# Kernel tuning notes

Hardware: AMD Instinct MI355X
Metric: run time of the kernel (lower is better)

## Reference

```python
import jax, jax.numpy as jnp
import numpy as np

NEG = -1e9  # effective -inf in log space (finite to keep grads NaN-free)


def _forward_lattice(theta, A):
    """alpha[b,i,j,s]: log-prob of all alignments reaching cell (i,j) in state s.
    States: 0=match (diag move), 1=insert-x (down move), 2=insert-y (right move).
    alpha[i,j,s] = theta[i,j,s] + LSE_k(alpha[i-ds,j-dj,k] + A[k,s]).
    Start: only the match contribution at (0,0) gets log-prob 0."""
    B, N, M, S = theta.shape
    j_is0 = (jnp.arange(M) == 0)  # [M]

    def row_step(prev_row, xs):
        theta_row, i = xs  # theta_row: [B, M, S]
        # diag predecessor alpha[i-1, j-1, :]
        diag = jnp.concatenate(
            [jnp.full((B, 1, S), NEG, theta_row.dtype), prev_row[:, :-1]], axis=1)
        lse_m = jax.nn.logsumexp(diag + A[:, None, :, 0], axis=-1)      # [B, M]
        lse_m = jnp.where((i == 0) & j_is0[None, :], 0.0, lse_m)        # start at (0,0)
        lse_x = jax.nn.logsumexp(prev_row + A[:, None, :, 1], axis=-1)  # [B, M]
        m_vals = theta_row[:, :, 0] + lse_m
        x_vals = theta_row[:, :, 1] + lse_x
        th_y = theta_row[:, :, 2]

        def col_step(left, cxs):
            # left: alpha[i, j-1, :] -> [B, S]
            m_j, x_j, ty_j = cxs  # each [B]
            y_j = ty_j + jax.nn.logsumexp(left + A[:, :, 2], axis=-1)
            cell = jnp.stack([m_j, x_j, y_j], axis=-1)  # [B, S]
            return cell, cell

        left0 = jnp.full((B, S), NEG, theta_row.dtype)
        _, row = jax.lax.scan(col_step, left0, (m_vals.T, x_vals.T, th_y.T))
        row = jnp.transpose(row, (1, 0, 2))  # [B, M, S]
        return row, row

    prev0 = jnp.full((B, M, S), NEG, theta.dtype)
    _, alpha = jax.lax.scan(row_step, prev0, (jnp.swapaxes(theta, 0, 1), jnp.arange(N)))
    return jnp.swapaxes(alpha, 0, 1)  # [B, N, M, S]


def _backward_lattice(theta, A):
    """beta[b,i,j,s]: log-prob of all alignment suffixes from (i,j) in state s.
    beta[i,j,s] = LSE( A[s,0]+theta[i+1,j+1,0]+beta[i+1,j+1,0],
                       A[s,1]+theta[i+1,j,1]  +beta[i+1,j,1],
                       A[s,2]+theta[i,j+1,2]  +beta[i,j+1,2] ),  beta[N-1,M-1,:] = 0.
    Computed as a forward scan on the flipped grid with u = beta + theta."""
    B, N, M, S = theta.shape
    theta_f = theta[:, ::-1, ::-1]
    j_is0 = (jnp.arange(M) == 0)

    def row_step(u_prev, xs):
        th_row, p = xs  # th_row: [B, M, S] (flipped coords)
        t_m = jnp.concatenate(
            [jnp.full((B, 1), NEG, th_row.dtype), u_prev[:, :-1, 0]], axis=1)  # [B, M]
        t_x = u_prev[:, :, 1]  # [B, M]

        def col_step(left_u2, cxs):
            tm_j, tx_j, th_j, j0 = cxs  # [B], [B], [B,S], scalar bool
            v = jnp.stack([tm_j, tx_j, left_u2], axis=-1)     # [B, S] over successor k
            g = jax.nn.logsumexp(A + v[:, None, :], axis=-1)  # [B, S]
            g = jnp.where((p == 0) & j0, 0.0, g)              # terminal cell
            u = g + th_j
            return u[:, 2], (g, u)

        left0 = jnp.full((B,), NEG, th_row.dtype)
        _, (g_row, u_row) = jax.lax.scan(
            col_step, left0, (t_m.T, t_x.T, jnp.swapaxes(th_row, 0, 1), j_is0))
        return jnp.transpose(u_row, (1, 0, 2)), jnp.transpose(g_row, (1, 0, 2))

    u0 = jnp.full((B, M, S), NEG, theta.dtype)
    _, g = jax.lax.scan(row_step, u0, (jnp.swapaxes(theta_f, 0, 1), jnp.arange(N)))
    g = jnp.swapaxes(g, 0, 1)  # [B, N, M, S] flipped coords
    return g[:, ::-1, ::-1]


def setup_inputs() -> dict:
    key = jax.random.key(0)
    k1, k2 = jax.random.split(key)
    B, N, M, S = 256, 128, 128, 3
    theta = jax.random.normal(k1, (B, N, M, S), dtype=jnp.float32)
    A = jax.random.normal(k2, (B, S, S), dtype=jnp.float32)
    return {"theta": theta, "A": A}


def reference(theta, A):
    # Baum-Welch: posterior log-marginals gamma = alpha + beta - logZ
    alpha = _forward_lattice(theta, A)
    beta = _backward_lattice(theta, A)
    logZ = jax.nn.logsumexp(alpha[:, -1, -1, :], axis=-1)  # [B]
    return alpha + beta - logZ[:, None, None, None]
```

## Files before the change

kernel.cpp:

```cpp
#include <hip/hip_runtime.h>

#define HNEG (-1000000000.0f)

constexpr int Nc = 128;
constexpr int Mc = 128;
constexpr int CELLS = Nc * Mc * 3;

__device__ __host__ constexpr int dpoff(int d) {
  return d <= 128 ? (d * (d + 1)) / 2 + ((d + 1) >> 1)
                  : 16448 - ((255 - d) * (256 - d)) / 2 + ((d - 127) >> 1);
}
__device__ __forceinline__ int dlod(int d) { return d > 127 ? d - 127 : 0; }
__device__ __forceinline__ int sidx(int d, int j) {
  const int lo = dlod(d);
  return dpoff(d) + j - lo + (lo & 1);
}
constexpr int PCELLS = 16512;
constexpr int PFLOATS = PCELLS * 3;
constexpr int AWSTRIDE = CELLS + 16;

__device__ __forceinline__ float lse3(float a, float b, float c) {
  float mx = fmaxf(fmaxf(a, b), c);
  return mx + __logf(__expf(a - mx) + __expf(b - mx) + __expf(c - mx));
}

__device__ __forceinline__ float shr1f(float src, float fill) {
  return __int_as_float(__builtin_amdgcn_update_dpp(
      __float_as_int(fill), __float_as_int(src), 0x138, 0xF, 0xF, false));
}

__device__ __forceinline__ void st3_even(float* o, float a, float b, float c) {
  *(float2*)o = make_float2(a, b);
  o[2] = c;
}
__device__ __forceinline__ void st3_odd(float* o, float a, float b, float c) {
  o[0] = a;
  *(float2*)(o + 1) = make_float2(b, c);
}

__global__ __launch_bounds__(256) void transpose_kernel(
    const float* __restrict__ theta, float* __restrict__ thd) {
  const int b = blockIdx.x;
  const int tile = blockIdx.y;
  const int i0 = (tile >> 1) * 64, j0 = (tile & 1) * 64;
  const int t = threadIdx.x;
  __shared__ float lds[64 * 192];
  float4* lds4 = (float4*)lds;
  const float4* src4 = (const float4*)(theta + (size_t)b * CELLS);
  float* dst = thd + (size_t)b * PFLOATS;
  const int cbase = (j0 >> 6) * 48;
  for (int f = t; f < 64 * 48; f += 256) {
    const int r = f / 48, c4 = f - r * 48;
    lds4[f] = src4[(size_t)(i0 + r) * 96 + cbase + c4];
  }
  __syncthreads();
  const int g = t >> 6, w = t & 63;
  for (int ld = g; ld < 127; ld += 4) {
    const int d = i0 + j0 + ld;
    const int ljlo = ld > 63 ? ld - 63 : 0;
    const int ljhi = ld < 63 ? ld : 63;
    const int L = (ljhi - ljlo + 1) * 3;
    const int base = sidx(d, j0 + ljlo) * 3;
    for (int e = w; e < L; e += 64) {
      const int lj = ljlo + e / 3, s = e - (e / 3) * 3;
      dst[base + e] = lds[(ld - lj) * 192 + lj * 3 + s];
    }
  }
}

#define DECL6(p) float p##0, p##1, p##2, p##3, p##4, p##5


#define F2LOAD(P, dd) do {                                                     \
    const int dc_ = (dd) > 254 ? 254 : (dd);                                   \
    const float2* p2_ = (const float2*)(thd + (size_t)sidx(dc_, jA) * 3);      \
    const float2 la_ = p2_[0], lb_ = p2_[1], lc_ = p2_[2];                     \
    P##0 = la_.x; P##1 = la_.y; P##2 = lb_.x;                                  \
    P##3 = lb_.y; P##4 = lc_.x; P##5 = lc_.y;                                  \
  } while (0)

#define F2STEP(P, dd) do {                                                     \
    const int iA_ = (dd) - jA, iB_ = (dd) - jB;                                \
    const bool okA_ = (unsigned)iA_ < (unsigned)Nc;                            \
    const bool okB_ = (unsigned)iB_ < (unsigned)Nc;                            \
    const float g0 = mS2 + __logf(wS20 * E00 + wS21 * E10 + wS22 * E20);       \
    const float g1 = mPA + __logf(wPA0 * E01 + wPA1 * E11 + wPA2 * E21);       \
    const float g2 = mS1 + __logf(wS10 * E02 + wS11 * E12 + wS12 * E22);       \
    const float cA0 = okA_ ? P##0 + g0 : HNEG;                                 \
    const float cA1 = okA_ ? P##1 + g1 : HNEG;                                 \
    const float cA2 = okA_ ? P##2 + g2 : HNEG;                                 \
    st3_even(okA_ ? aw + (iA_ * Mc + jA) * 3 : dmpE, cA0, cA1, cA2);           \
    const float h0 = mPP + __logf(wPP0 * E00 + wPP1 * E10 + wPP2 * E20);       \
    const float h1 = mPB + __logf(wPB0 * E01 + wPB1 * E11 + wPB2 * E21);       \
    const float h2 = mPA + __logf(wPA0 * E02 + wPA1 * E12 + wPA2 * E22);       \
    const float cB0 = okB_ ? P##3 + h0 : HNEG;                                 \
    const float cB1 = okB_ ? P##4 + h1 : HNEG;                                 \
    const float cB2 = okB_ ? P##5 + h2 : HNEG;                                 \
    st3_odd(okB_ ? aw + (iB_ * Mc + jB) * 3 : dmpO, cB0, cB1, cB2);            \
    const float mA_ = fmaxf(fmaxf(cA0, cA1), cA2);                             \
    const float a0_ = __expf(cA0 - mA_), a1_ = __expf(cA1 - mA_),              \
                a2_ = __expf(cA2 - mA_);                                       \
    const float mB_ = fmaxf(fmaxf(cB0, cB1), cB2);                             \
    const float b0_ = __expf(cB0 - mB_), b1_ = __expf(cB1 - mB_),              \
                b2_ = __expf(cB2 - mB_);                                       \
    mPP = mPA; wPP0 = wPA0; wPP1 = wPA1; wPP2 = wPA2;                          \
    mPA = mA_; wPA0 = a0_; wPA1 = a1_; wPA2 = a2_;                             \
    mPB = mB_; wPB0 = b0_; wPB1 = b1_; wPB2 = b2_;                             \
    mS2 = mS1; wS20 = wS10; wS21 = wS11; wS22 = wS12;                          \
    mS1 = shr1f(mB_, HNEG);                                                    \
    wS10 = shr1f(b0_, 1.f); wS11 = shr1f(b1_, 1.f); wS12 = shr1f(b2_, 1.f);    \
  } while (0)

#define B2LOADL(Pt, dd) do {                                                   \
    int dor_ = 254 - (dd); if (dor_ < 0) dor_ = 0;                             \
    const float2* p2_ = (const float2*)(thd + (size_t)sidx(dor_, jjB) * 3);    \
    const float2 la_ = p2_[0], lb_ = p2_[1], lc_ = p2_[2];                     \
    Pt##3 = la_.x; Pt##4 = la_.y; Pt##5 = lb_.x;                               \
    Pt##0 = lb_.y; Pt##1 = lc_.x; Pt##2 = lc_.y;                               \
  } while (0)

#define B2STEPL(Pt, dd) do {                                                   \
    const int iA_ = Nc - 1 - (dd) + jA;                                        \
    const int iB_ = Nc - 1 - (dd) + jB;                                        \
    const bool okA_ = (unsigned)iA_ < (unsigned)Nc;                            \
    const bool okB_ = (unsigned)iB_ < (unsigned)Nc;                            \
    float uA0, uA1, uA2, uB0, uB1, uB2;                                        \
    {                                                                          \
      const float v0 = S2u0, v1 = pAu1, v2 = S1u2;                             \
      const float mv = fmaxf(fmaxf(v0, v1), v2);                               \
      const float w0 = __expf(v0 - mv), w1 = __expf(v1 - mv),                  \
                  w2 = __expf(v2 - mv);                                        \
      float g0 = mv + __logf(w0 * E00 + w1 * E01 + w2 * E02);                  \
      float g1 = mv + __logf(w0 * E10 + w1 * E11 + w2 * E12);                  \
      float g2 = mv + __logf(w0 * E20 + w1 * E21 + w2 * E22);                  \
      if ((dd) == 0 && l == 0) { g0 = 0.f; g1 = 0.f; g2 = 0.f; }               \
      uA0 = okA_ ? g0 + Pt##0 : HNEG;                                          \
      uA1 = okA_ ? g1 + Pt##1 : HNEG;                                          \
      uA2 = okA_ ? g2 + Pt##2 : HNEG;                                          \
      st3_odd(okA_ ? ob + (iA_ * Mc + jjA) * 3 : dmpO, g0, g1, g2);            \
    }                                                                          \
    {                                                                          \
      const float v0 = ppAu0, v1 = pBu1, v2 = pAu2;                            \
      const float mv = fmaxf(fmaxf(v0, v1), v2);                               \
      const float w0 = __expf(v0 - mv), w1 = __expf(v1 - mv),                  \
                  w2 = __expf(v2 - mv);                                        \
      const float g0 = mv + __logf(w0 * E00 + w1 * E01 + w2 * E02);            \
      const float g1 = mv + __logf(w0 * E10 + w1 * E11 + w2 * E12);            \
      const float g2 = mv + __logf(w0 * E20 + w1 * E21 + w2 * E22);            \
      uB0 = okB_ ? g0 + Pt##3 : HNEG;                                          \
      uB1 = okB_ ? g1 + Pt##4 : HNEG;                                          \
      uB2 = okB_ ? g2 + Pt##5 : HNEG;                                          \
      st3_even(okB_ ? ob + (iB_ * Mc + jjB) * 3 : dmpE, g0, g1, g2);           \
    }                                                                          \
    ppAu0 = pAu0; pAu0 = uA0; pAu1 = uA1; pAu2 = uA2; pBu1 = uB1;              \
    S2u0 = S1u0;                                                               \
    S1u0 = shr1f(uB0, HNEG);                                                   \
    S1u2 = shr1f(uB2, HNEG);                                                   \
  } while (0)

__global__ __launch_bounds__(128, 1) void fb2_kernel(
    const float* __restrict__ thd_, const float* __restrict__ A,
    float* __restrict__ aw_, float* __restrict__ logZ_ws,
    float* __restrict__ ob_) {
  const int b = blockIdx.x;
  const int wave = threadIdx.x >> 6;
  const int l = threadIdx.x & 63;
  const float* thd = thd_ + (size_t)b * PFLOATS;
  const float* Ab = A + b * 9;
  const float E00 = __expf(Ab[0]), E01 = __expf(Ab[1]), E02 = __expf(Ab[2]);
  const float E10 = __expf(Ab[3]), E11 = __expf(Ab[4]), E12 = __expf(Ab[5]);
  const float E20 = __expf(Ab[6]), E21 = __expf(Ab[7]), E22 = __expf(Ab[8]);

  const int jA = 2 * l, jB = 2 * l + 1;
  float* dpad = aw_ + (size_t)b * AWSTRIDE + CELLS;

  if (wave == 0) {
    float* aw = aw_ + (size_t)b * AWSTRIDE;
    float* dmpE = dpad;
    float* dmpO = dpad + 3;

    float mPA = HNEG, wPA0 = 1.f, wPA1 = 1.f, wPA2 = 1.f;
    float mPB = HNEG, wPB0 = 1.f, wPB1 = 1.f, wPB2 = 1.f;
    float mPP = HNEG, wPP0 = 1.f, wPP1 = 1.f, wPP2 = 1.f;
    float mS1 = HNEG, wS10 = 1.f, wS11 = 1.f, wS12 = 1.f;
    float mS2 = HNEG, wS20 = 1.f, wS21 = 1.f, wS22 = 1.f;
    if (l == 0) { mS2 = 0.f; wS20 = 1.0f / E00; wS21 = 0.f; wS22 = 0.f; }

    DECL6(xt0); DECL6(xt1); DECL6(xt2); DECL6(xt3);
    DECL6(yt0); DECL6(yt1); DECL6(yt2); DECL6(yt3);

    F2LOAD(xt0, 0); F2LOAD(xt1, 1); F2LOAD(xt2, 2); F2LOAD(xt3, 3);
    F2LOAD(yt0, 4); F2LOAD(yt1, 5); F2LOAD(yt2, 6); F2LOAD(yt3, 7);

    for (int t = 0; t < 31; ++t) {
      const int d0 = 8 * t;
      F2STEP(xt0, d0 + 0); F2STEP(xt1, d0 + 1); F2STEP(xt2, d0 + 2); F2STEP(xt3, d0 + 3);
      F2LOAD(xt0, d0 + 8); F2LOAD(xt1, d0 + 9); F2LOAD(xt2, d0 + 10); F2LOAD(xt3, d0 + 11);
      F2STEP(yt0, d0 + 4); F2STEP(yt1, d0 + 5); F2STEP(yt2, d0 + 6); F2STEP(yt3, d0 + 7);
      F2LOAD(yt0, d0 + 12); F2LOAD(yt1, d0 + 13); F2LOAD(yt2, d0 + 14); F2LOAD(yt3, d0 + 15);
    }
    F2STEP(xt0, 248); F2STEP(xt1, 249); F2STEP(xt2, 250); F2STEP(xt3, 251);
    F2STEP(yt0, 252); F2STEP(yt1, 253); F2STEP(yt2, 254);
    if (l == 63) logZ_ws[b] = mPB + __logf(wPB0 + wPB1 + wPB2);
  } else {
    float* ob = ob_ + (size_t)b * CELLS;
    const int jjA = Mc - 1 - jA, jjB = Mc - 1 - jB;
    float* dmpE = dpad + 8;
    float* dmpO = dpad + 11;

    float pAu0 = HNEG, pAu1 = HNEG, pAu2 = HNEG;
    float ppAu0 = HNEG, pBu1 = HNEG;
    float S1u0 = HNEG, S1u2 = HNEG, S2u0 = HNEG;

    DECL6(xt0); DECL6(xt1); DECL6(xt2); DECL6(xt3);
    DECL6(yt0); DECL6(yt1); DECL6(yt2); DECL6(yt3);

    B2LOADL(xt0, 0); B2LOADL(xt1, 1); B2LOADL(xt2, 2); B2LOADL(xt3, 3);
    B2LOADL(yt0, 4); B2LOADL(yt1, 5); B2LOADL(yt2, 6); B2LOADL(yt3, 7);

    for (int t = 0; t < 31; ++t) {
      const int d0 = 8 * t;
      B2STEPL(xt0, d0 + 0); B2STEPL(xt1, d0 + 1);
      B2STEPL(xt2, d0 + 2); B2STEPL(xt3, d0 + 3);
      B2LOADL(xt0, d0 + 8); B2LOADL(xt1, d0 + 9);
      B2LOADL(xt2, d0 + 10); B2LOADL(xt3, d0 + 11);
      B2STEPL(yt0, d0 + 4); B2STEPL(yt1, d0 + 5);
      B2STEPL(yt2, d0 + 6); B2STEPL(yt3, d0 + 7);
      B2LOADL(yt0, d0 + 12); B2LOADL(yt1, d0 + 13);
      B2LOADL(yt2, d0 + 14); B2LOADL(yt3, d0 + 15);
    }
    B2STEPL(xt0, 248); B2STEPL(xt1, 249); B2STEPL(xt2, 250); B2STEPL(xt3, 251);
    B2STEPL(yt0, 252); B2STEPL(yt1, 253); B2STEPL(yt2, 254);
  }
}

__global__ __launch_bounds__(256) void combine_kernel(
    const float4* __restrict__ aw4, const float* __restrict__ logZ_ws,
    float4* __restrict__ out4) {
  const int b = blockIdx.x;
  const float lz = logZ_ws[b];
  const int off = blockIdx.y * 1024 + threadIdx.x;
  const size_t ab = (size_t)b * (AWSTRIDE / 4);
  const size_t obx = (size_t)b * 12288;
#pragma unroll
  for (int k = 0; k < 4; ++k) {
    const size_t i = off + (size_t)k * 256;
    const float4 a = aw4[ab + i];
    const float4 g = out4[obx + i];
    out4[obx + i] = make_float4(a.x + g.x - lz, a.y + g.y - lz,
                                a.z + g.z - lz, a.w + g.w - lz);
  }
}

__global__ __launch_bounds__(128) void fwd_fb(const float* __restrict__ theta,
                                              const float* __restrict__ A,
                                              float* __restrict__ out) {
  const int b = blockIdx.x;
  const int j = threadIdx.x;
  const float* th = theta + (size_t)b * CELLS;
  float* ob = out + (size_t)b * CELLS;

  __shared__ float sA[9];
  __shared__ float ring[3][Mc + 1][3];
  if (j < 9) sA[j] = A[b * 9 + j];
  {
    float* rf = &ring[0][0][0];
    for (int t = j; t < 3 * (Mc + 1) * 3; t += Mc) rf[t] = HNEG;
  }
  __syncthreads();
  const float A00 = sA[0], A01 = sA[1], A02 = sA[2];
  const float A10 = sA[3], A11 = sA[4], A12 = sA[5];
  const float A20 = sA[6], A21 = sA[7], A22 = sA[8];

  float p0 = HNEG, p1 = HNEG, p2 = HNEG;
  float tc0 = 0.f, tc1 = 0.f, tc2 = 0.f, tn0 = 0.f, tn1 = 0.f, tn2 = 0.f;
  if (j == 0) { tc0 = th[0]; tc1 = th[1]; tc2 = th[2]; }
  if (j <= 1) {
    const int i1 = 1 - j;
    const float* p = th + (i1 * Mc + j) * 3;
    tn0 = p[0]; tn1 = p[1]; tn2 = p[2];
  }
  int s0 = 0, s1 = 2, s2 = 1;
  for (int d = 0; d < Nc + Mc - 1; ++d) {
    const int i = d - j;
    float tf0 = 0.f, tf1 = 0.f, tf2 = 0.f;
    const int ip = i + 2;
    if (ip >= 0 && ip < Nc) {
      const float* p = th + (ip * Mc + j) * 3;
      tf0 = p[0]; tf1 = p[1]; tf2 = p[2];
    }
    float c0 = HNEG, c1 = HNEG, c2 = HNEG;
    if (i >= 0 && i < Nc) {
      const float* nd1 = ring[s1][j];
      const float* nd2 = ring[s2][j];
      float lm = lse3(nd2[0] + A00, nd2[1] + A10, nd2[2] + A20);
      if (i == 0 && j == 0) lm = 0.0f;
      float lx = lse3(p0 + A01, p1 + A11, p2 + A21);
      float ly = lse3(nd1[0] + A02, nd1[1] + A12, nd1[2] + A22);
      c0 = tc0 + lm; c1 = tc1 + lx; c2 = tc2 + ly;
      float* o = ob + (i * Mc + j) * 3;
      o[0] = c0; o[1] = c1; o[2] = c2;
    }
    float* w = ring[s0][j + 1];
    w[0] = c0; w[1] = c1; w[2] = c2;
    __syncthreads();
    p0 = c0; p1 = c1; p2 = c2;
    tc0 = tn0; tc1 = tn1; tc2 = tn2;
    tn0 = tf0; tn1 = tf1; tn2 = tf2;
    const int t = s2; s2 = s1; s1 = s0; s0 = t;
  }
}

__global__ __launch_bounds__(128) void bwd_fb(const float* __restrict__ theta,
                                              const float* __restrict__ A,
                                              float* __restrict__ ob_) {
  const int b = blockIdx.x;
  const int q = threadIdx.x;
  const float* th = theta + (size_t)b * CELLS;
  float* ob = ob_ + (size_t)b * CELLS;

  __shared__ float sA[9];
  __shared__ float ring[3][Mc + 1][3];
  __shared__ float sZ;
  if (q < 9) sA[q] = A[b * 9 + q];
  {
    float* rf = &ring[0][0][0];
    for (int t = q; t < 3 * (Mc + 1) * 3; t += Mc) rf[t] = HNEG;
  }
  if (q == 0) {
    sZ = lse3(ob[(Nc * Mc - 1) * 3 + 0], ob[(Nc * Mc - 1) * 3 + 1],
              ob[(Nc * Mc - 1) * 3 + 2]);
  }
  __syncthreads();
  const float A00 = sA[0], A01 = sA[1], A02 = sA[2];
  const float A10 = sA[3], A11 = sA[4], A12 = sA[5];
  const float A20 = sA[6], A21 = sA[7], A22 = sA[8];
  const float logZ = sZ;

  const int jj = Mc - 1 - q;
  float pu1 = HNEG;
  float tc0 = 0.f, tc1 = 0.f, tc2 = 0.f, tn0 = 0.f, tn1 = 0.f, tn2 = 0.f;
  float ac0 = 0.f, ac1 = 0.f, ac2 = 0.f, an0 = 0.f, an1 = 0.f, an2 = 0.f;
  if (q == 0) {
    const float* p = th + ((Nc - 1) * Mc + jj) * 3;
    tc0 = p[0]; tc1 = p[1]; tc2 = p[2];
    const float* a = ob + ((Nc - 1) * Mc + jj) * 3;
    ac0 = a[0]; ac1 = a[1]; ac2 = a[2];
  }
  if (q <= 1) {
    const int i1 = Nc - 2 + q;
    const float* p = th + (i1 * Mc + jj) * 3;
    tn0 = p[0]; tn1 = p[1]; tn2 = p[2];
    const float* a = ob + (i1 * Mc + jj) * 3;
    an0 = a[0]; an1 = a[1]; an2 = a[2];
  }
  int s0 = 0, s1 = 2, s2 = 1;
  for (int d = 0; d < Nc + Mc - 1; ++d) {
    const int p = d - q;
    const int i = Nc - 1 - p;
    float tf0 = 0.f, tf1 = 0.f, tf2 = 0.f, af0 = 0.f, af1 = 0.f, af2 = 0.f;
    const int ipf = i - 2;
    if (ipf >= 0 && ipf < Nc) {
      const float* pp = th + (ipf * Mc + jj) * 3;
      tf0 = pp[0]; tf1 = pp[1]; tf2 = pp[2];
      const float* aa = ob + (ipf * Mc + jj) * 3;
      af0 = aa[0]; af1 = aa[1]; af2 = aa[2];
    }
    float u0 = HNEG, u1 = HNEG, u2 = HNEG;
    if (p >= 0 && p < Nc) {
      const float* nd1 = ring[s1][q];
      const float* nd2 = ring[s2][q];
      const float v0 = nd2[0];
      const float v1 = pu1;
      const float v2 = nd1[2];
      float g0 = lse3(A00 + v0, A01 + v1, A02 + v2);
      float g1 = lse3(A10 + v0, A11 + v1, A12 + v2);
      float g2 = lse3(A20 + v0, A21 + v1, A22 + v2);
      if (p == 0 && q == 0) { g0 = 0.0f; g1 = 0.0f; g2 = 0.0f; }
      u0 = g0 + tc0; u1 = g1 + tc1; u2 = g2 + tc2;
      float* o = ob + (i * Mc + jj) * 3;
      o[0] = ac0 + g0 - logZ;
      o[1] = ac1 + g1 - logZ;
      o[2] = ac2 + g2 - logZ;
    }
    float* w = ring[s0][q + 1];
    w[0] = u0; w[1] = u1; w[2] = u2;
    __syncthreads();
    pu1 = u1;
    tc0 = tn0; tc1 = tn1; tc2 = tn2;
    tn0 = tf0; tn1 = tf1; tn2 = tf2;
    ac0 = an0; ac1 = an1; ac2 = an2;
    an0 = af0; an1 = af1; an2 = af2;
    const int t = s2; s2 = s1; s1 = s0; s0 = t;
  }
}

extern "C" void kernel_launch(void* const* d_in, const int* in_sizes, int n_in,
                              void* d_out, int out_size, void* d_ws, size_t ws_size,
                              hipStream_t stream) {
  const float* theta = (const float*)d_in[0];
  const float* A = (const float*)d_in[1];
  float* out = (float*)d_out;
  const int B = in_sizes[1] / 9;

  const size_t need = (size_t)B * (PFLOATS + AWSTRIDE + 1) * 4;
  if (ws_size >= need) {
    float* thd = (float*)d_ws;
    float* aw = thd + (size_t)B * PFLOATS;
    float* logZ_ws = aw + (size_t)B * AWSTRIDE;
    transpose_kernel<<<dim3(B, 4), dim3(256), 0, stream>>>(theta, thd);
    fb2_kernel<<<dim3(B), dim3(128), 0, stream>>>(thd, A, aw, logZ_ws, out);
    combine_kernel<<<dim3(B, 12), dim3(256), 0, stream>>>(
        (const float4*)aw, logZ_ws, (float4*)out);
  } else {
    fwd_fb<<<dim3(B), dim3(128), 0, stream>>>(theta, A, out);
    bwd_fb<<<dim3(B), dim3(128), 0, stream>>>(theta, A, out);
  }
}
```

Measured before the change: 240.3 us.

## Run lattice recurrences in base-2 log space and use uniform theta addressing

The theta repack pre-scales values by 1/ln2, so both forward and backward recurrences can use the native exp2/log2 instructions in place of __expf/__logf, which each carry an extra multiply. The final combine multiplies by ln2 to return to natural log. Theta load addresses are also computed once per wave with readfirstlane plus a per-lane offset, moving index arithmetic to scalar registers. This adds rounding from the scaling and relies on the repack's lane layout matching the per-lane offset.

```diff
diff --git a/kernel.cpp b/kernel.cpp
--- a/kernel.cpp
+++ b/kernel.cpp
@@ -1,10 +1,20 @@
 #include <hip/hip_runtime.h>
 
 #define HNEG (-1000000000.0f)
+#define HNEG2 (-1.44269504e9f)
+#define INVLN2 1.44269504088896341f
+#define LN2F 0.69314718055994531f
 
 constexpr int Nc = 128;
 constexpr int Mc = 128;
 constexpr int CELLS = Nc * Mc * 3;
+
+__device__ __forceinline__ float ex2(float x) {
+  return __builtin_amdgcn_exp2f(x);
+}
+__device__ __forceinline__ float lg2(float x) {
+  return __builtin_amdgcn_logf(x);
+}
 
 __device__ __host__ constexpr int dpoff(int d) {
   return d <= 128 ? (d * (d + 1)) / 2 + ((d + 1) >> 1)
@@ -14,6 +24,10 @@
 __device__ __forceinline__ int sidx(int d, int j) {
   const int lo = dlod(d);
   return dpoff(d) + j - lo + (lo & 1);
+}
+__device__ __forceinline__ int sidx_u(int d) {
+  const int lo = dlod(d);
+  return dpoff(d) - lo + (lo & 1);
 }
 constexpr int PCELLS = 16512;
 constexpr int PFLOATS = PCELLS * 3;
@@ -63,7 +77,7 @@
     const int base = sidx(d, j0 + ljlo) * 3;
     for (int e = w; e < L; e += 64) {
       const int lj = ljlo + e / 3, s = e - (e / 3) * 3;
-      dst[base + e] = lds[(ld - lj) * 192 + lj * 3 + s];
+      dst[base + e] = lds[(ld - lj) * 192 + lj * 3 + s] * INVLN2;
     }
   }
 }
@@ -73,7 +87,8 @@
 
 #define F2LOAD(P, dd) do {                                                     \
     const int dc_ = (dd) > 254 ? 254 : (dd);                                   \
-    const float2* p2_ = (const float2*)(thd + (size_t)sidx(dc_, jA) * 3);      \
+    const int su_ = __builtin_amdgcn_readfirstlane(sidx_u(dc_));               \
+    const float2* p2_ = (const float2*)thd + ((su_ * 3) >> 1) + 3 * l;         \
     const float2 la_ = p2_[0], lb_ = p2_[1], lc_ = p2_[2];                     \
     P##0 = la_.x; P##1 = la_.y; P##2 = lb_.x;                                  \
     P##3 = lb_.y; P##4 = lc_.x; P##5 = lc_.y;                                  \
@@ -83,37 +98,39 @@
     const int iA_ = (dd) - jA, iB_ = (dd) - jB;                                \
     const bool okA_ = (unsigned)iA_ < (unsigned)Nc;                            \
     const bool okB_ = (unsigned)iB_ < (unsigned)Nc;                            \
-    const float g0 = mS2 + __logf(wS20 * E00 + wS21 * E10 + wS22 * E20);       \
-    const float g1 = mPA + __logf(wPA0 * E01 + wPA1 * E11 + wPA2 * E21);       \
-    const float g2 = mS1 + __logf(wS10 * E02 + wS11 * E12 + wS12 * E22);       \
-    const float cA0 = okA_ ? P##0 + g0 : HNEG;                                 \
-    const float cA1 = okA_ ? P##1 + g1 : HNEG;                                 \
-    const float cA2 = okA_ ? P##2 + g2 : HNEG;                                 \
+    const float g0 = mS2 + lg2(wS20 * E00 + wS21 * E10 + wS22 * E20);          \
+    const float g1 = mPA + lg2(wPA0 * E01 + wPA1 * E11 + wPA2 * E21);          \
+    const float g2 = mS1 + lg2(wS10 * E02 + wS11 * E12 + wS12 * E22);          \
+    const float cA0 = okA_ ? P##0 + g0 : HNEG2;                                \
+    const float cA1 = okA_ ? P##1 + g1 : HNEG2;                                \
+    const float cA2 = okA_ ? P##2 + g2 : HNEG2;                                \
     st3_even(okA_ ? aw + (iA_ * Mc + jA) * 3 : dmpE, cA0, cA1, cA2);           \
-    const float h0 = mPP + __logf(wPP0 * E00 + wPP1 * E10 + wPP2 * E20);       \
-    const float h1 = mPB + __logf(wPB0 * E01 + wPB1 * E11 + wPB2 * E21);       \
-    const float h2 = mPA + __logf(wPA0 * E02 + wPA1 * E12 + wPA2 * E22);       \
-    const float cB0 = okB_ ? P##3 + h0 : HNEG;                                 \
-    const float cB1 = okB_ ? P##4 + h1 : HNEG;                                 \
-    const float cB2 = okB_ ? P##5 + h2 : HNEG;                                 \
+    const float h0 = mPP + lg2(wPP0 * E00 + wPP1 * E10 + wPP2 * E20);          \
+    const float h1 = mPB + lg2(wPB0 * E01 + wPB1 * E11 + wPB2 * E21);          \
+    const float h2 = mPA + lg2(wPA0 * E02 + wPA1 * E12 + wPA2 * E22);          \
+    const float cB0 = okB_ ? P##3 + h0 : HNEG2;                                \
+    const float cB1 = okB_ ? P##4 + h1 : HNEG2;                                \
+    const float cB2 = okB_ ? P##5 + h2 : HNEG2;                                \
     st3_odd(okB_ ? aw + (iB_ * Mc + jB) * 3 : dmpO, cB0, cB1, cB2);            \
     const float mA_ = fmaxf(fmaxf(cA0, cA1), cA2);                             \
-    const float a0_ = __expf(cA0 - mA_), a1_ = __expf(cA1 - mA_),              \
-                a2_ = __expf(cA2 - mA_);                                       \
+    const float a0_ = ex2(cA0 - mA_), a1_ = ex2(cA1 - mA_),                    \
+                a2_ = ex2(cA2 - mA_);                                          \
     const float mB_ = fmaxf(fmaxf(cB0, cB1), cB2);                             \
-    const float b0_ = __expf(cB0 - mB_), b1_ = __expf(cB1 - mB_),              \
-                b2_ = __expf(cB2 - mB_);                                       \
+    const float b0_ = ex2(cB0 - mB_), b1_ = ex2(cB1 - mB_),                    \
+                b2_ = ex2(cB2 - mB_);                                          \
     mPP = mPA; wPP0 = wPA0; wPP1 = wPA1; wPP2 = wPA2;                          \
     mPA = mA_; wPA0 = a0_; wPA1 = a1_; wPA2 = a2_;                             \
     mPB = mB_; wPB0 = b0_; wPB1 = b1_; wPB2 = b2_;                             \
     mS2 = mS1; wS20 = wS10; wS21 = wS11; wS22 = wS12;                          \
-    mS1 = shr1f(mB_, HNEG);                                                    \
+    mS1 = shr1f(mB_, HNEG2);                                                   \
     wS10 = shr1f(b0_, 1.f); wS11 = shr1f(b1_, 1.f); wS12 = shr1f(b2_, 1.f);    \
   } while (0)
 
 #define B2LOADL(Pt, dd) do {                                                   \
     int dor_ = 254 - (dd); if (dor_ < 0) dor_ = 0;                             \
-    const float2* p2_ = (const float2*)(thd + (size_t)sidx(dor_, jjB) * 3);    \
+    const int su_ = __builtin_amdgcn_readfirstlane(sidx_u(dor_));              \
+    const float2* p2_ =                                                        \
+        (const float2*)thd + ((su_ * 3) >> 1) + 3 * (63 - l);                  \
     const float2 la_ = p2_[0], lb_ = p2_[1], lc_ = p2_[2];                     \
     Pt##3 = la_.x; Pt##4 = la_.y; Pt##5 = lb_.x;                               \
     Pt##0 = lb_.y; Pt##1 = lc_.x; Pt##2 = lc_.y;                               \
@@ -128,34 +145,32 @@
     {                                                                          \
       const float v0 = S2u0, v1 = pAu1, v2 = S1u2;                             \
       const float mv = fmaxf(fmaxf(v0, v1), v2);                               \
-      const float w0 = __expf(v0 - mv), w1 = __expf(v1 - mv),                  \
-                  w2 = __expf(v2 - mv);                                        \
-      float g0 = mv + __logf(w0 * E00 + w1 * E01 + w2 * E02);                  \
-      float g1 = mv + __logf(w0 * E10 + w1 * E11 + w2 * E12);                  \
-      float g2 = mv + __logf(w0 * E20 + w1 * E21 + w2 * E22);                  \
+      const float w0 = ex2(v0 - mv), w1 = ex2(v1 - mv), w2 = ex2(v2 - mv);     \
+      float g0 = mv + lg2(w0 * E00 + w1 * E01 + w2 * E02);                     \
+      float g1 = mv + lg2(w0 * E10 + w1 * E11 + w2 * E12);                     \
+      float g2 = mv + lg2(w0 * E20 + w1 * E21 + w2 * E22);                     \
       if ((dd) == 0 && l == 0) { g0 = 0.f; g1 = 0.f; g2 = 0.f; }               \
-      uA0 = okA_ ? g0 + Pt##0 : HNEG;                                          \
-      uA1 = okA_ ? g1 + Pt##1 : HNEG;                                          \
-      uA2 = okA_ ? g2 + Pt##2 : HNEG;                                          \
+      uA0 = okA_ ? g0 + Pt##0 : HNEG2;                                         \
+      uA1 = okA_ ? g1 + Pt##1 : HNEG2;                                         \
+      uA2 = okA_ ? g2 + Pt##2 : HNEG2;                                         \
       st3_odd(okA_ ? ob + (iA_ * Mc + jjA) * 3 : dmpO, g0, g1, g2);            \
     }                                                                          \
     {                                                                          \
       const float v0 = ppAu0, v1 = pBu1, v2 = pAu2;                            \
       const float mv = fmaxf(fmaxf(v0, v1), v2);                               \
-      const float w0 = __expf(v0 - mv), w1 = __expf(v1 - mv),                  \
-                  w2 = __expf(v2 - mv);                                        \
-      const float g0 = mv + __logf(w0 * E00 + w1 * E01 + w2 * E02);            \
-      const float g1 = mv + __logf(w0 * E10 + w1 * E11 + w2 * E12);            \
-      const float g2 = mv + __logf(w0 * E20 + w1 * E21 + w2 * E22);            \
-      uB0 = okB_ ? g0 + Pt##3 : HNEG;                                          \
-      uB1 = okB_ ? g1 + Pt##4 : HNEG;                                          \
-      uB2 = okB_ ? g2 + Pt##5 : HNEG;                                          \
+      const float w0 = ex2(v0 - mv), w1 = ex2(v1 - mv), w2 = ex2(v2 - mv);     \
+      const float g0 = mv + lg2(w0 * E00 + w1 * E01 + w2 * E02);               \
+      const float g1 = mv + lg2(w0 * E10 + w1 * E11 + w2 * E12);               \
+      const float g2 = mv + lg2(w0 * E20 + w1 * E21 + w2 * E22);               \
+      uB0 = okB_ ? g0 + Pt##3 : HNEG2;                                         \
+      uB1 = okB_ ? g1 + Pt##4 : HNEG2;                                         \
+      uB2 = okB_ ? g2 + Pt##5 : HNEG2;                                         \
       st3_even(okB_ ? ob + (iB_ * Mc + jjB) * 3 : dmpE, g0, g1, g2);           \
     }                                                                          \
     ppAu0 = pAu0; pAu0 = uA0; pAu1 = uA1; pAu2 = uA2; pBu1 = uB1;              \
     S2u0 = S1u0;                                                               \
-    S1u0 = shr1f(uB0, HNEG);                                                   \
-    S1u2 = shr1f(uB2, HNEG);                                                   \
+    S1u0 = shr1f(uB0, HNEG2);                                                  \
+    S1u2 = shr1f(uB2, HNEG2);                                                  \
   } while (0)
 
 __global__ __launch_bounds__(128, 1) void fb2_kernel(
@@ -179,11 +194,11 @@
     float* dmpE = dpad;
     float* dmpO = dpad + 3;
 
-    float mPA = HNEG, wPA0 = 1.f, wPA1 = 1.f, wPA2 = 1.f;
-    float mPB = HNEG, wPB0 = 1.f, wPB1 = 1.f, wPB2 = 1.f;
-    float mPP = HNEG, wPP0 = 1.f, wPP1 = 1.f, wPP2 = 1.f;
-    float mS1 = HNEG, wS10 = 1.f, wS11 = 1.f, wS12 = 1.f;
-    float mS2 = HNEG, wS20 = 1.f, wS21 = 1.f, wS22 = 1.f;
+    float mPA = HNEG2, wPA0 = 1.f, wPA1 = 1.f, wPA2 = 1.f;
+    float mPB = HNEG2, wPB0 = 1.f, wPB1 = 1.f, wPB2 = 1.f;
+    float mPP = HNEG2, wPP0 = 1.f, wPP1 = 1.f, wPP2 = 1.f;
+    float mS1 = HNEG2, wS10 = 1.f, wS11 = 1.f, wS12 = 1.f;
+    float mS2 = HNEG2, wS20 = 1.f, wS21 = 1.f, wS22 = 1.f;
     if (l == 0) { mS2 = 0.f; wS20 = 1.0f / E00; wS21 = 0.f; wS22 = 0.f; }
 
     DECL6(xt0); DECL6(xt1); DECL6(xt2); DECL6(xt3);
@@ -201,16 +216,16 @@
     }
     F2STEP(xt0, 248); F2STEP(xt1, 249); F2STEP(xt2, 250); F2STEP(xt3, 251);
     F2STEP(yt0, 252); F2STEP(yt1, 253); F2STEP(yt2, 254);
-    if (l == 63) logZ_ws[b] = mPB + __logf(wPB0 + wPB1 + wPB2);
+    if (l == 63) logZ_ws[b] = mPB + lg2(wPB0 + wPB1 + wPB2);
   } else {
     float* ob = ob_ + (size_t)b * CELLS;
     const int jjA = Mc - 1 - jA, jjB = Mc - 1 - jB;
     float* dmpE = dpad + 8;
     float* dmpO = dpad + 11;
 
-    float pAu0 = HNEG, pAu1 = HNEG, pAu2 = HNEG;
-    float ppAu0 = HNEG, pBu1 = HNEG;
-    float S1u0 = HNEG, S1u2 = HNEG, S2u0 = HNEG;
+    float pAu0 = HNEG2, pAu1 = HNEG2, pAu2 = HNEG2;
+    float ppAu0 = HNEG2, pBu1 = HNEG2;
+    float S1u0 = HNEG2, S1u2 = HNEG2, S2u0 = HNEG2;
 
     DECL6(xt0); DECL6(xt1); DECL6(xt2); DECL6(xt3);
     DECL6(yt0); DECL6(yt1); DECL6(yt2); DECL6(yt3);
@@ -247,8 +262,9 @@
     const size_t i = off + (size_t)k * 256;
     const float4 a = aw4[ab + i];
     const float4 g = out4[obx + i];
-    out4[obx + i] = make_float4(a.x + g.x - lz, a.y + g.y - lz,
-                                a.z + g.z - lz, a.w + g.w - lz);
+    out4[obx + i] =
+        make_float4((a.x + g.x - lz) * LN2F, (a.y + g.y - lz) * LN2F,
+                    (a.z + g.z - lz) * LN2F, (a.w + g.w - lz) * LN2F);
   }
 }
 
```

After: 204.0 us, median of 2. -15.1%, faster.
